# Optimization experiments

Hardware: AMD Instinct MI355X
Metric: run time of the kernel (lower is better)

Reference implementation:

```python
import jax, jax.numpy as jnp
import numpy as np

B, N, K = 4, 32768, 16
IN_DIM, HID, OUT_DIM = 32, 64, 32
N_DIM = 2
KIN = 2 * N_DIM + OUT_DIM  # 36
KH = 64
EPS = 1e-5


def _gelu(x):
    return jax.nn.gelu(x, approximate=False)  # torch F.gelu default (erf)


def setup_inputs() -> dict:
    key = jax.random.key(0)
    ks = jax.random.split(key, 16)
    s = lambda fan_in: 1.0 / np.sqrt(fan_in)
    return {
        "inp": jax.random.normal(ks[0], (B, N, IN_DIM), jnp.float32),
        "input_grid": jax.random.uniform(ks[1], (N, N_DIM), jnp.float32),
        "output_grid": jax.random.uniform(ks[2], (N, N_DIM), jnp.float32),
        "neighbor_idx": jax.random.randint(ks[3], (N, K), 0, N, jnp.int32),
        # pointwise projection MLP: in_dim -> hid -> out_dim, GELU between
        "Wp1": jax.random.normal(ks[4], (IN_DIM, HID), jnp.float32) * s(IN_DIM),
        "bp1": jnp.zeros((HID,), jnp.float32),
        "Wp2": jax.random.normal(ks[5], (HID, OUT_DIM), jnp.float32) * s(HID),
        "bp2": jnp.zeros((OUT_DIM,), jnp.float32),
        # per-edge kernel MLP: [2*n_dim+out_dim, 64, 64, out_dim], GELU between
        "Wk1": jax.random.normal(ks[6], (KIN, KH), jnp.float32) * s(KIN),
        "bk1": jnp.zeros((KH,), jnp.float32),
        "Wk2": jax.random.normal(ks[7], (KH, KH), jnp.float32) * s(KH),
        "bk2": jnp.zeros((KH,), jnp.float32),
        "Wk3": jax.random.normal(ks[8], (KH, OUT_DIM), jnp.float32) * s(KH),
        "bk3": jnp.zeros((OUT_DIM,), jnp.float32),
        # LayerNorm
        "ln_gamma": jnp.ones((OUT_DIM,), jnp.float32),
        "ln_beta": jnp.zeros((OUT_DIM,), jnp.float32),
    }


def reference(inp, input_grid, output_grid, neighbor_idx,
              Wp1, bp1, Wp2, bp2, Wk1, bk1, Wk2, bk2, Wk3, bk3,
              ln_gamma, ln_beta):
    # pointwise projection MLP
    x = _gelu(jnp.einsum('bnc,ch->bnh', inp, Wp1) + bp1)
    x = jnp.einsum('bnh,ho->bno', x, Wp2) + bp2  # (B, N, OUT_DIM)

    # neighbor gather (fixed K neighbors per output point)
    f_y = x[:, neighbor_idx, :]                      # (B, N, K, C)
    y_pos = input_grid[neighbor_idx]                 # (N, K, n_dim)
    x_pos = jnp.broadcast_to(output_grid[:, None, :], (N, K, N_DIM))
    pos_feat = jnp.concatenate([y_pos, x_pos], axis=-1)          # (N, K, 2*n_dim)
    agg = jnp.concatenate(
        [jnp.broadcast_to(pos_feat[None], (x.shape[0], N, K, 2 * N_DIM)), f_y],
        axis=-1)                                      # (B, N, K, KIN)

    # nonlinear kernel MLP k(x, y, f(y))
    h = _gelu(jnp.einsum('bnkc,ch->bnkh', agg, Wk1) + bk1)
    h = _gelu(jnp.einsum('bnkh,hg->bnkg', h, Wk2) + bk2)
    k_out = jnp.einsum('bnkg,go->bnko', h, Wk3) + bk3  # (B, N, K, OUT_DIM)

    # mean-aggregate over neighbors (integral transform)
    out = jnp.mean(k_out, axis=2)                      # (B, N, OUT_DIM)

    # residual (shapes match) + LayerNorm over channels
    out = out + x
    mu = jnp.mean(out, axis=-1, keepdims=True)
    var = jnp.mean((out - mu) ** 2, axis=-1, keepdims=True)
    out = (out - mu) * jax.lax.rsqrt(var + EPS) * ln_gamma + ln_beta
    return out
```

## Files before the change

kernel.cpp:

```cpp
#include <hip/hip_runtime.h>
#include <hip/hip_bf16.h>

#define BB 4
#define NN 32768
#define KKN 16
#define IN_DIM 32
#define HID 64
#define OUT_DIM 32
#define KH 64
#define WS 88
#define TOT (BB * NN)
#define NWAVES 8192
#define GTAB_N 4096

typedef __bf16 bf16;
typedef float f32x4 __attribute__((ext_vector_type(4)));
typedef bf16 bf16x8 __attribute__((ext_vector_type(8)));
typedef bf16 bf16x4 __attribute__((ext_vector_type(4)));

__device__ __forceinline__ float gelu_f(float x) {
    float x2 = x * x;
    float t  = x * fmaf(0.10294358f, x2, 2.3022082f);
    float E  = __builtin_amdgcn_exp2f(t);
    float r  = __builtin_amdgcn_rcpf(E + 1.0f);
    return fmaf(-x, r, x);
}

__global__ __launch_bounds__(256) void point_mlp_kernel(
    const float* __restrict__ inp, const float* __restrict__ Wp1,
    const float* __restrict__ bp1, const float* __restrict__ Wp2,
    const float* __restrict__ bp2, bf16* __restrict__ xbf)
{
    __shared__ __align__(16) bf16 hb[4][16 * WS];
    const int tid = threadIdx.x, w = tid >> 6, lane = tid & 63;
    const int q = lane >> 4, nl = lane & 15;

    bf16x8 w1f[4];
    #pragma unroll
    for (int nb = 0; nb < 4; nb++)
        #pragma unroll
        for (int j = 0; j < 8; j++)
            w1f[nb][j] = (bf16)Wp1[(q * 8 + j) * HID + nb * 16 + nl];
    bf16x8 w2f[2][2];
    #pragma unroll
    for (int nb = 0; nb < 2; nb++)
        #pragma unroll
        for (int c = 0; c < 2; c++)
            #pragma unroll
            for (int j = 0; j < 8; j++) {
                int k = c * 32 + q * 8 + j, kp = ((k & 3) << 4) | (k >> 2);
                w2f[nb][c][j] = (bf16)Wp2[kp * OUT_DIM + nb * 16 + nl];
            }
    float b1v[4], b2v[2];
    #pragma unroll
    for (int nb = 0; nb < 4; nb++) b1v[nb] = bp1[nb * 16 + nl];
    b2v[0] = bp2[nl]; b2v[1] = bp2[16 + nl];

    const int gw = blockIdx.x * 4 + w;
    const int nw = gridDim.x * 4;

    for (int t = gw; t < TOT / 16; t += nw) {
        const int R = t * 16;
        const float* ap = inp + (size_t)(R + nl) * IN_DIM + q * 8;
        float4 av0 = *(const float4*)ap, av1 = *(const float4*)(ap + 4);
        bf16x8 af;
        af[0] = (bf16)av0.x; af[1] = (bf16)av0.y; af[2] = (bf16)av0.z; af[3] = (bf16)av0.w;
        af[4] = (bf16)av1.x; af[5] = (bf16)av1.y; af[6] = (bf16)av1.z; af[7] = (bf16)av1.w;

        f32x4 acc[4];
        #pragma unroll
        for (int nb = 0; nb < 4; nb++)
            acc[nb] = (f32x4){b1v[nb], b1v[nb], b1v[nb], b1v[nb]};
        #pragma unroll
        for (int nb = 0; nb < 4; nb++)
            acc[nb] = __builtin_amdgcn_mfma_f32_16x16x32_bf16(af, w1f[nb], acc[nb], 0, 0, 0);

        #pragma unroll
        for (int r = 0; r < 4; r++) {
            bf16x4 hv;
            #pragma unroll
            for (int nb = 0; nb < 4; nb++) hv[nb] = (bf16)gelu_f(acc[nb][r]);
            *(bf16x4*)&hb[w][(q * 4 + r) * WS + nl * 4] = hv;
        }
        bf16x8 a0 = *(const bf16x8*)&hb[w][nl * WS + q * 8];
        bf16x8 a1 = *(const bf16x8*)&hb[w][nl * WS + 32 + q * 8];
        f32x4 a2[2];
        #pragma unroll
        for (int nb = 0; nb < 2; nb++) {
            a2[nb] = (f32x4){b2v[nb], b2v[nb], b2v[nb], b2v[nb]};
            a2[nb] = __builtin_amdgcn_mfma_f32_16x16x32_bf16(a0, w2f[nb][0], a2[nb], 0, 0, 0);
            a2[nb] = __builtin_amdgcn_mfma_f32_16x16x32_bf16(a1, w2f[nb][1], a2[nb], 0, 0, 0);
        }
        #pragma unroll
        for (int r = 0; r < 4; r++)
            #pragma unroll
            for (int nb = 0; nb < 2; nb++)
                xbf[(size_t)(R + q * 4 + r) * OUT_DIM + nb * 16 + nl] = (bf16)a2[nb][r];
    }
}

__global__ __launch_bounds__(256) void gnn_edge_kernel(
    const bf16*  __restrict__ xbf,
    const float* __restrict__ igrid, const float* __restrict__ ogrid,
    const int*   __restrict__ nbi,
    const float* __restrict__ Wk1, const float* __restrict__ bk1,
    const float* __restrict__ Wk2, const float* __restrict__ bk2,
    const float* __restrict__ Wk3, const float* __restrict__ bk3,
    const float* __restrict__ gma, const float* __restrict__ bta,
    float* __restrict__ out)
{
    __shared__ __align__(16) bf16 tile[8][16 * WS];
    __shared__ __align__(16) bf16 gtab[GTAB_N];

    const int tid = threadIdx.x, w = tid >> 6, lane = tid & 63;
    const int q = lane >> 4, nl = lane & 15;
    bf16* __restrict__ TA = tile[w * 2];
    bf16* __restrict__ TB = tile[w * 2 + 1];

    for (int i = tid; i < GTAB_N; i += 256) {
        float x = (float)i * 0.0078125f - 16.0f;
        gtab[i] = (bf16)(0.5f * x * (1.0f + erff(x * 0.70710678f)));
    }

    bf16x8 w1f[4][2], w2f[4][2], w3f[2][2];
    #pragma unroll
    for (int nb = 0; nb < 4; nb++) {
        #pragma unroll
        for (int j = 0; j < 8; j++) {
            w1f[nb][0][j] = (bf16)Wk1[(4 + q * 8 + j) * KH + nb * 16 + nl];
            float v1 = 0.0f;
            if (j < 4 && q == 0) v1 = Wk1[j * KH + nb * 16 + nl];
            w1f[nb][1][j] = (bf16)v1;
        }
        #pragma unroll
        for (int c = 0; c < 2; c++)
            #pragma unroll
            for (int j = 0; j < 8; j++) {
                int k = c * 32 + q * 8 + j, kp = ((k & 3) << 4) | (k >> 2);
                w2f[nb][c][j] = (bf16)Wk2[kp * KH + nb * 16 + nl];
            }
    }
    #pragma unroll
    for (int nb = 0; nb < 2; nb++)
        #pragma unroll
        for (int c = 0; c < 2; c++)
            #pragma unroll
            for (int j = 0; j < 8; j++) {
                int k = c * 32 + q * 8 + j, kp = ((k & 3) << 4) | (k >> 2);
                w3f[nb][c][j] = (bf16)Wk3[kp * OUT_DIM + nb * 16 + nl];
            }

    float b1v[4], b2v[4], b3v[2];
    #pragma unroll
    for (int nb = 0; nb < 4; nb++) { b1v[nb] = bk1[nb * 16 + nl]; b2v[nb] = bk2[nb * 16 + nl]; }
    b3v[0] = bk3[nl]; b3v[1] = bk3[16 + nl];
    const float g0 = gma[nl], g1 = gma[16 + nl], be0 = bta[nl], be1 = bta[16 + nl];

    const int gw = blockIdx.x * 4 + w;
    const int e = lane >> 2, part = lane & 3;

    {
        const bf16x8 zf = {(bf16)0.f,(bf16)0.f,(bf16)0.f,(bf16)0.f,(bf16)0.f,(bf16)0.f,(bf16)0.f,(bf16)0.f};
        for (int i = lane * 8; i < 16 * WS; i += 64 * 8) { *(bf16x8*)&TA[i] = zf; *(bf16x8*)&TB[i] = zf; }
    }
    __syncthreads();

    #define GLUT(x) gtab[(unsigned)fminf(fmaxf(fmaf((x), 128.0f, 2048.5f), 0.0f), 4095.0f)]

    int tA = gw, tB = gw + NWAVES;
    int nA = nbi[(tA & (NN - 1)) * KKN + e];
    int nB = nbi[(tB & (NN - 1)) * KKN + e];
    uint4 fyA = ((const uint4*)(xbf + ((size_t)((tA >> 15) * NN + nA)) * OUT_DIM))[part];
    uint4 fyB = ((const uint4*)(xbf + ((size_t)((tB >> 15) * NN + nB)) * OUT_DIM))[part];
    float2 ipA, opA, ipB, opB;
    if (part == 0) {
        ipA = ((const float2*)igrid)[nA]; opA = ((const float2*)ogrid)[tA & (NN - 1)];
        ipB = ((const float2*)igrid)[nB]; opB = ((const float2*)ogrid)[tB & (NN - 1)];
    }
    bf16 xA0 = xbf[(size_t)tA * OUT_DIM + nl],      xA1 = xbf[(size_t)tA * OUT_DIM + 16 + nl];
    bf16 xB0 = xbf[(size_t)tB * OUT_DIM + nl],      xB1 = xbf[(size_t)tB * OUT_DIM + 16 + nl];

    #pragma unroll 1
    for (int it = 0; it < TOT / (2 * NWAVES); ++it) {
        *(uint4*)&TA[e * WS + part * 8] = fyA;
        *(uint4*)&TB[e * WS + part * 8] = fyB;
        if (part == 0) {
            bf16x4 pA = {(bf16)ipA.x, (bf16)ipA.y, (bf16)opA.x, (bf16)opA.y};
            bf16x4 pB = {(bf16)ipB.x, (bf16)ipB.y, (bf16)opB.x, (bf16)opB.y};
            *(bf16x4*)&TA[e * WS + 32] = pA;
            *(bf16x4*)&TB[e * WS + 32] = pB;
        }
        const float rA0 = (float)xA0, rA1 = (float)xA1, rB0 = (float)xB0, rB1 = (float)xB1;

        const int tA2 = (tA + 2 * NWAVES) & (TOT - 1);
        const int tB2 = tA2 + NWAVES;
        const int nA2 = nbi[(tA2 & (NN - 1)) * KKN + e];
        const int nB2 = nbi[(tB2 & (NN - 1)) * KKN + e];

        bf16x8 aA0 = *(const bf16x8*)&TA[nl * WS + q * 8];
        bf16x8 aA1 = *(const bf16x8*)&TA[nl * WS + 32 + q * 8];
        bf16x8 aB0 = *(const bf16x8*)&TB[nl * WS + q * 8];
        bf16x8 aB1 = *(const bf16x8*)&TB[nl * WS + 32 + q * 8];
        f32x4 cA[4], cB[4];
        #pragma unroll
        for (int nb = 0; nb < 4; nb++) {
            cA[nb] = (f32x4){b1v[nb], b1v[nb], b1v[nb], b1v[nb]};
            cB[nb] = (f32x4){b1v[nb], b1v[nb], b1v[nb], b1v[nb]};
        }
        #pragma unroll
        for (int nb = 0; nb < 4; nb++) {
            cA[nb] = __builtin_amdgcn_mfma_f32_16x16x32_bf16(aA0, w1f[nb][0], cA[nb], 0, 0, 0);
            cB[nb] = __builtin_amdgcn_mfma_f32_16x16x32_bf16(aB0, w1f[nb][0], cB[nb], 0, 0, 0);
            cA[nb] = __builtin_amdgcn_mfma_f32_16x16x32_bf16(aA1, w1f[nb][1], cA[nb], 0, 0, 0);
            cB[nb] = __builtin_amdgcn_mfma_f32_16x16x32_bf16(aB1, w1f[nb][1], cB[nb], 0, 0, 0);
        }
        #pragma unroll
        for (int r = 0; r < 4; r++) {
            bf16x4 hA, hB;
            #pragma unroll
            for (int nb = 0; nb < 4; nb++) {
                hA[nb] = GLUT(cA[nb][r]);
                hB[nb] = GLUT(cB[nb][r]);
            }
            *(bf16x4*)&TA[(q * 4 + r) * WS + nl * 4] = hA;
            *(bf16x4*)&TB[(q * 4 + r) * WS + nl * 4] = hB;
        }

        uint4 fyA2 = ((const uint4*)(xbf + ((size_t)((tA2 >> 15) * NN + nA2)) * OUT_DIM))[part];
        uint4 fyB2 = ((const uint4*)(xbf + ((size_t)((tB2 >> 15) * NN + nB2)) * OUT_DIM))[part];
        float2 ipA2, opA2, ipB2, opB2;
        if (part == 0) {
            ipA2 = ((const float2*)igrid)[nA2]; opA2 = ((const float2*)ogrid)[tA2 & (NN - 1)];
            ipB2 = ((const float2*)igrid)[nB2]; opB2 = ((const float2*)ogrid)[tB2 & (NN - 1)];
        }
        bf16 xA0n = xbf[(size_t)tA2 * OUT_DIM + nl],  xA1n = xbf[(size_t)tA2 * OUT_DIM + 16 + nl];
        bf16 xB0n = xbf[(size_t)tB2 * OUT_DIM + nl],  xB1n = xbf[(size_t)tB2 * OUT_DIM + 16 + nl];

        aA0 = *(const bf16x8*)&TA[nl * WS + q * 8];
        aA1 = *(const bf16x8*)&TA[nl * WS + 32 + q * 8];
        aB0 = *(const bf16x8*)&TB[nl * WS + q * 8];
        aB1 = *(const bf16x8*)&TB[nl * WS + 32 + q * 8];
        #pragma unroll
        for (int nb = 0; nb < 4; nb++) {
            cA[nb] = (f32x4){b2v[nb], b2v[nb], b2v[nb], b2v[nb]};
            cB[nb] = (f32x4){b2v[nb], b2v[nb], b2v[nb], b2v[nb]};
        }
        #pragma unroll
        for (int nb = 0; nb < 4; nb++) {
            cA[nb] = __builtin_amdgcn_mfma_f32_16x16x32_bf16(aA0, w2f[nb][0], cA[nb], 0, 0, 0);
            cB[nb] = __builtin_amdgcn_mfma_f32_16x16x32_bf16(aB0, w2f[nb][0], cB[nb], 0, 0, 0);
            cA[nb] = __builtin_amdgcn_mfma_f32_16x16x32_bf16(aA1, w2f[nb][1], cA[nb], 0, 0, 0);
            cB[nb] = __builtin_amdgcn_mfma_f32_16x16x32_bf16(aB1, w2f[nb][1], cB[nb], 0, 0, 0);
        }
        #pragma unroll
        for (int r = 0; r < 4; r++) {
            bf16x4 hA, hB;
            #pragma unroll
            for (int nb = 0; nb < 4; nb++) {
                hA[nb] = GLUT(cA[nb][r]);
                hB[nb] = GLUT(cB[nb][r]);
            }
            *(bf16x4*)&TA[(q * 4 + r) * WS + nl * 4] = hA;
            *(bf16x4*)&TB[(q * 4 + r) * WS + nl * 4] = hB;
        }

        aA0 = *(const bf16x8*)&TA[nl * WS + q * 8];
        aA1 = *(const bf16x8*)&TA[nl * WS + 32 + q * 8];
        aB0 = *(const bf16x8*)&TB[nl * WS + q * 8];
        aB1 = *(const bf16x8*)&TB[nl * WS + 32 + q * 8];
        f32x4 dA[2], dB[2];
        #pragma unroll
        for (int nb = 0; nb < 2; nb++) {
            dA[nb] = (f32x4){0.f, 0.f, 0.f, 0.f};
            dB[nb] = (f32x4){0.f, 0.f, 0.f, 0.f};
            dA[nb] = __builtin_amdgcn_mfma_f32_16x16x32_bf16(aA0, w3f[nb][0], dA[nb], 0, 0, 0);
            dB[nb] = __builtin_amdgcn_mfma_f32_16x16x32_bf16(aB0, w3f[nb][0], dB[nb], 0, 0, 0);
            dA[nb] = __builtin_amdgcn_mfma_f32_16x16x32_bf16(aA1, w3f[nb][1], dA[nb], 0, 0, 0);
            dB[nb] = __builtin_amdgcn_mfma_f32_16x16x32_bf16(aB1, w3f[nb][1], dB[nb], 0, 0, 0);
        }

        {
            float s0 = dA[0][0] + dA[0][1] + dA[0][2] + dA[0][3];
            float s1 = dA[1][0] + dA[1][1] + dA[1][2] + dA[1][3];
            float u0 = dB[0][0] + dB[0][1] + dB[0][2] + dB[0][3];
            float u1 = dB[1][0] + dB[1][1] + dB[1][2] + dB[1][3];
            s0 += __shfl_xor(s0, 16, 64); s0 += __shfl_xor(s0, 32, 64);
            s1 += __shfl_xor(s1, 16, 64); s1 += __shfl_xor(s1, 32, 64);
            u0 += __shfl_xor(u0, 16, 64); u0 += __shfl_xor(u0, 32, 64);
            u1 += __shfl_xor(u1, 16, 64); u1 += __shfl_xor(u1, 32, 64);

            float oA0 = s0 * 0.0625f + b3v[0] + rA0;
            float oA1 = s1 * 0.0625f + b3v[1] + rA1;
            float oB0 = u0 * 0.0625f + b3v[0] + rB0;
            float oB1 = u1 * 0.0625f + b3v[1] + rB1;

            float mA = oA0 + oA1, mB = oB0 + oB1;
            mA += __shfl_xor(mA, 1, 64); mB += __shfl_xor(mB, 1, 64);
            mA += __shfl_xor(mA, 2, 64); mB += __shfl_xor(mB, 2, 64);
            mA += __shfl_xor(mA, 4, 64); mB += __shfl_xor(mB, 4, 64);
            mA += __shfl_xor(mA, 8, 64); mB += __shfl_xor(mB, 8, 64);
            mA *= (1.0f / 32.0f); mB *= (1.0f / 32.0f);
            float dA0 = oA0 - mA, dA1 = oA1 - mA, dB0 = oB0 - mB, dB1 = oB1 - mB;
            float vA = dA0 * dA0 + dA1 * dA1, vB = dB0 * dB0 + dB1 * dB1;
            vA += __shfl_xor(vA, 1, 64); vB += __shfl_xor(vB, 1, 64);
            vA += __shfl_xor(vA, 2, 64); vB += __shfl_xor(vB, 2, 64);
            vA += __shfl_xor(vA, 4, 64); vB += __shfl_xor(vB, 4, 64);
            vA += __shfl_xor(vA, 8, 64); vB += __shfl_xor(vB, 8, 64);
            float rsA = rsqrtf(vA * (1.0f / 32.0f) + 1e-5f);
            float rsB = rsqrtf(vB * (1.0f / 32.0f) + 1e-5f);

            if (q == 0) {
                float* oa = out + (size_t)tA * OUT_DIM;
                float* ob = out + (size_t)tB * OUT_DIM;
                oa[nl]      = fmaf(dA0 * rsA, g0, be0);
                oa[16 + nl] = fmaf(dA1 * rsA, g1, be1);
                ob[nl]      = fmaf(dB0 * rsB, g0, be0);
                ob[16 + nl] = fmaf(dB1 * rsB, g1, be1);
            }
        }

        tA = tA2; tB = tB2;
        fyA = fyA2; fyB = fyB2;
        ipA = ipA2; opA = opA2; ipB = ipB2; opB = opB2;
        xA0 = xA0n; xA1 = xA1n; xB0 = xB0n; xB1 = xB1n;
    }
    #undef GLUT
}

extern "C" void kernel_launch(void* const* d_in, const int* in_sizes, int n_in,
                              void* d_out, int out_size, void* d_ws, size_t ws_size,
                              hipStream_t stream) {
    const float* inp   = (const float*)d_in[0];
    const float* igrid = (const float*)d_in[1];
    const float* ogrid = (const float*)d_in[2];
    const int*   nbi   = (const int*)d_in[3];
    const float* Wp1   = (const float*)d_in[4];
    const float* bp1   = (const float*)d_in[5];
    const float* Wp2   = (const float*)d_in[6];
    const float* bp2   = (const float*)d_in[7];
    const float* Wk1   = (const float*)d_in[8];
    const float* bk1   = (const float*)d_in[9];
    const float* Wk2   = (const float*)d_in[10];
    const float* bk2   = (const float*)d_in[11];
    const float* Wk3   = (const float*)d_in[12];
    const float* bk3   = (const float*)d_in[13];
    const float* gma   = (const float*)d_in[14];
    const float* bta   = (const float*)d_in[15];
    float* out = (float*)d_out;
    bf16* xbf = (bf16*)d_ws;

    point_mlp_kernel<<<1024, 256, 0, stream>>>(inp, Wp1, bp1, Wp2, bp2, xbf);
    gnn_edge_kernel<<<2048, 256, 0, stream>>>(xbf, igrid, ogrid, nbi,
                                              Wk1, bk1, Wk2, bk2, Wk3, bk3,
                                              gma, bta, out);
}
```

Baseline: 215.8 us.

## Move edge-MLP weight fragments to LDS, raise occupancy, use DPP row reductions

Stores the pre-permuted Wk2/Wk3 bf16 MFMA fragments in shared memory instead of holding them in registers, reloading them from LDS inside the loop. It also requests 3 blocks per SM through launch bounds. Together these free VGPRs so more waves can stay resident and hide gather latency. The LayerNorm mean/variance 16-lane reductions now use DPP quad_perm/row_ror adds instead of shfl_xor. The trade-off is extra LDS traffic and LDS footprint on every iteration, on top of existing GELU-table lookups.

```diff
diff --git a/kernel.cpp b/kernel.cpp
--- a/kernel.cpp
+++ b/kernel.cpp
@@ -26,6 +26,21 @@
     return fmaf(-x, r, x);
 }
 
+template <int CTRL>
+__device__ __forceinline__ float dppadd(float v) {
+    union { float f; int i; } u, r;
+    u.f = v;
+    r.i = __builtin_amdgcn_update_dpp(0, u.i, CTRL, 0xf, 0xf, true);
+    return v + r.f;
+}
+__device__ __forceinline__ float rowsum16(float v) {
+    v = dppadd<0xB1>(v);
+    v = dppadd<0x4E>(v);
+    v = dppadd<0x124>(v);
+    v = dppadd<0x128>(v);
+    return v;
+}
+
 __global__ __launch_bounds__(256) void point_mlp_kernel(
     const float* __restrict__ inp, const float* __restrict__ Wp1,
     const float* __restrict__ bp1, const float* __restrict__ Wp2,
@@ -99,7 +114,7 @@
     }
 }
 
-__global__ __launch_bounds__(256) void gnn_edge_kernel(
+__global__ __launch_bounds__(256, 3) void gnn_edge_kernel(
     const bf16*  __restrict__ xbf,
     const float* __restrict__ igrid, const float* __restrict__ ogrid,
     const int*   __restrict__ nbi,
@@ -111,6 +126,8 @@
 {
     __shared__ __align__(16) bf16 tile[8][16 * WS];
     __shared__ __align__(16) bf16 gtab[GTAB_N];
+    __shared__ __align__(16) bf16 w2s[8 * 64 * 8];
+    __shared__ __align__(16) bf16 w3s[4 * 64 * 8];
 
     const int tid = threadIdx.x, w = tid >> 6, lane = tid & 63;
     const int q = lane >> 4, nl = lane & 15;
@@ -121,8 +138,28 @@
         float x = (float)i * 0.0078125f - 16.0f;
         gtab[i] = (bf16)(0.5f * x * (1.0f + erff(x * 0.70710678f)));
     }
-
-    bf16x8 w1f[4][2], w2f[4][2], w3f[2][2];
+    for (int idx = tid; idx < 8 * 64; idx += 256) {
+        int f = idx >> 6, l = idx & 63;
+        int fnb = f >> 1, fc = f & 1, fq = l >> 4, fnl = l & 15;
+        bf16x8 v;
+        #pragma unroll
+        for (int j = 0; j < 8; j++) {
+            int k = fc * 32 + fq * 8 + j, kp = ((k & 3) << 4) | (k >> 2);
+            v[j] = (bf16)Wk2[kp * KH + fnb * 16 + fnl];
+        }
+        *(bf16x8*)&w2s[idx * 8] = v;
+        if (f < 4) {
+            bf16x8 v3;
+            #pragma unroll
+            for (int j = 0; j < 8; j++) {
+                int k = fc * 32 + fq * 8 + j, kp = ((k & 3) << 4) | (k >> 2);
+                v3[j] = (bf16)Wk3[kp * OUT_DIM + fnb * 16 + fnl];
+            }
+            *(bf16x8*)&w3s[idx * 8] = v3;
+        }
+    }
+
+    bf16x8 w1f[4][2];
     #pragma unroll
     for (int nb = 0; nb < 4; nb++) {
         #pragma unroll
@@ -132,23 +169,7 @@
             if (j < 4 && q == 0) v1 = Wk1[j * KH + nb * 16 + nl];
             w1f[nb][1][j] = (bf16)v1;
         }
-        #pragma unroll
-        for (int c = 0; c < 2; c++)
-            #pragma unroll
-            for (int j = 0; j < 8; j++) {
-                int k = c * 32 + q * 8 + j, kp = ((k & 3) << 4) | (k >> 2);
-                w2f[nb][c][j] = (bf16)Wk2[kp * KH + nb * 16 + nl];
-            }
-    }
-    #pragma unroll
-    for (int nb = 0; nb < 2; nb++)
-        #pragma unroll
-        for (int c = 0; c < 2; c++)
-            #pragma unroll
-            for (int j = 0; j < 8; j++) {
-                int k = c * 32 + q * 8 + j, kp = ((k & 3) << 4) | (k >> 2);
-                w3f[nb][c][j] = (bf16)Wk3[kp * OUT_DIM + nb * 16 + nl];
-            }
+    }
 
     float b1v[4], b2v[4], b3v[2];
     #pragma unroll
@@ -247,10 +268,12 @@
         }
         #pragma unroll
         for (int nb = 0; nb < 4; nb++) {
-            cA[nb] = __builtin_amdgcn_mfma_f32_16x16x32_bf16(aA0, w2f[nb][0], cA[nb], 0, 0, 0);
-            cB[nb] = __builtin_amdgcn_mfma_f32_16x16x32_bf16(aB0, w2f[nb][0], cB[nb], 0, 0, 0);
-            cA[nb] = __builtin_amdgcn_mfma_f32_16x16x32_bf16(aA1, w2f[nb][1], cA[nb], 0, 0, 0);
-            cB[nb] = __builtin_amdgcn_mfma_f32_16x16x32_bf16(aB1, w2f[nb][1], cB[nb], 0, 0, 0);
+            bf16x8 wf0 = *(const bf16x8*)&w2s[((nb * 2 + 0) * 64 + lane) * 8];
+            bf16x8 wf1 = *(const bf16x8*)&w2s[((nb * 2 + 1) * 64 + lane) * 8];
+            cA[nb] = __builtin_amdgcn_mfma_f32_16x16x32_bf16(aA0, wf0, cA[nb], 0, 0, 0);
+            cB[nb] = __builtin_amdgcn_mfma_f32_16x16x32_bf16(aB0, wf0, cB[nb], 0, 0, 0);
+            cA[nb] = __builtin_amdgcn_mfma_f32_16x16x32_bf16(aA1, wf1, cA[nb], 0, 0, 0);
+            cB[nb] = __builtin_amdgcn_mfma_f32_16x16x32_bf16(aB1, wf1, cB[nb], 0, 0, 0);
         }
         #pragma unroll
         for (int r = 0; r < 4; r++) {
@@ -271,12 +294,14 @@
         f32x4 dA[2], dB[2];
         #pragma unroll
         for (int nb = 0; nb < 2; nb++) {
+            bf16x8 wf0 = *(const bf16x8*)&w3s[((nb * 2 + 0) * 64 + lane) * 8];
+            bf16x8 wf1 = *(const bf16x8*)&w3s[((nb * 2 + 1) * 64 + lane) * 8];
             dA[nb] = (f32x4){0.f, 0.f, 0.f, 0.f};
             dB[nb] = (f32x4){0.f, 0.f, 0.f, 0.f};
-            dA[nb] = __builtin_amdgcn_mfma_f32_16x16x32_bf16(aA0, w3f[nb][0], dA[nb], 0, 0, 0);
-            dB[nb] = __builtin_amdgcn_mfma_f32_16x16x32_bf16(aB0, w3f[nb][0], dB[nb], 0, 0, 0);
-            dA[nb] = __builtin_amdgcn_mfma_f32_16x16x32_bf16(aA1, w3f[nb][1], dA[nb], 0, 0, 0);
-            dB[nb] = __builtin_amdgcn_mfma_f32_16x16x32_bf16(aB1, w3f[nb][1], dB[nb], 0, 0, 0);
+            dA[nb] = __builtin_amdgcn_mfma_f32_16x16x32_bf16(aA0, wf0, dA[nb], 0, 0, 0);
+            dB[nb] = __builtin_amdgcn_mfma_f32_16x16x32_bf16(aB0, wf0, dB[nb], 0, 0, 0);
+            dA[nb] = __builtin_amdgcn_mfma_f32_16x16x32_bf16(aA1, wf1, dA[nb], 0, 0, 0);
+            dB[nb] = __builtin_amdgcn_mfma_f32_16x16x32_bf16(aB1, wf1, dB[nb], 0, 0, 0);
         }
 
         {
@@ -294,20 +319,13 @@
             float oB0 = u0 * 0.0625f + b3v[0] + rB0;
             float oB1 = u1 * 0.0625f + b3v[1] + rB1;
 
-            float mA = oA0 + oA1, mB = oB0 + oB1;
-            mA += __shfl_xor(mA, 1, 64); mB += __shfl_xor(mB, 1, 64);
-            mA += __shfl_xor(mA, 2, 64); mB += __shfl_xor(mB, 2, 64);
-            mA += __shfl_xor(mA, 4, 64); mB += __shfl_xor(mB, 4, 64);
-            mA += __shfl_xor(mA, 8, 64); mB += __shfl_xor(mB, 8, 64);
-            mA *= (1.0f / 32.0f); mB *= (1.0f / 32.0f);
+            float mA = rowsum16(oA0 + oA1) * (1.0f / 32.0f);
+            float mB = rowsum16(oB0 + oB1) * (1.0f / 32.0f);
             float dA0 = oA0 - mA, dA1 = oA1 - mA, dB0 = oB0 - mB, dB1 = oB1 - mB;
-            float vA = dA0 * dA0 + dA1 * dA1, vB = dB0 * dB0 + dB1 * dB1;
-            vA += __shfl_xor(vA, 1, 64); vB += __shfl_xor(vB, 1, 64);
-            vA += __shfl_xor(vA, 2, 64); vB += __shfl_xor(vB, 2, 64);
-            vA += __shfl_xor(vA, 4, 64); vB += __shfl_xor(vB, 4, 64);
-            vA += __shfl_xor(vA, 8, 64); vB += __shfl_xor(vB, 8, 64);
-            float rsA = rsqrtf(vA * (1.0f / 32.0f) + 1e-5f);
-            float rsB = rsqrtf(vB * (1.0f / 32.0f) + 1e-5f);
+            float vA = rowsum16(dA0 * dA0 + dA1 * dA1) * (1.0f / 32.0f);
+            float vB = rowsum16(dB0 * dB0 + dB1 * dB1) * (1.0f / 32.0f);
+            float rsA = rsqrtf(vA + 1e-5f);
+            float rsB = rsqrtf(vB + 1e-5f);
 
             if (q == 0) {
                 float* oa = out + (size_t)tA * OUT_DIM;
```

Measured after the change: 298.7 us. 1.38x slower.
